# Kernel tuning notes

Measured on AMD Instinct MI355X. Metric: run time of the kernel, lower is better.

The kernel has to match this reference:

```python
import jax, jax.numpy as jnp
import numpy as np
from jax import lax

EPS = 1e-5

def bn(x, g, b):
    # training-mode BatchNorm2d over (N, H, W)
    m = jnp.mean(x, axis=(0, 2, 3), keepdims=True)
    v = jnp.var(x, axis=(0, 2, 3), keepdims=True)
    return (x - m) * lax.rsqrt(v + EPS) * g[None, :, None, None] + b[None, :, None, None]

def conv1x1(x, W):
    # x: [b,c,h,w], W: [o,c]
    return jnp.einsum('bchw,oc->bohw', x, W)

def conv3x3(x, W):
    # W: [o,i,3,3]
    return lax.conv_general_dilated(x, W, (1, 1), 'SAME',
                                    dimension_numbers=('NCHW', 'OIHW', 'NCHW'))

def lga(x, Wqkv, Wproj, g, b):
    # LinearGlobalAttention: O(N) global attention
    bsz, c, h, w = x.shape
    qkv = conv1x1(x, Wqkv)                       # [b, 3c, h, w]
    q, k, v = jnp.split(qkv, 3, axis=1)
    q = q.reshape(bsz, c, h * w)                 # [b, c, N]
    k = jax.nn.softmax(k.reshape(bsz, c, h * w), axis=-1)
    v = v.reshape(bsz, c, h * w)
    ctx = jnp.einsum('bcn,bdn->bcd', k, v)       # [b, c, c]
    out = jnp.einsum('bcd,bcn->bdn', ctx, q)     # context^T @ q -> [b, c, N]
    out = out.reshape(bsz, c, h, w)
    return jax.nn.relu(bn(conv1x1(out, Wproj), g, b))


def setup_inputs() -> dict:
    key = jax.random.key(0)
    ks = jax.random.split(key, 12)
    B, Cin, Cout, H, W = 16, 128, 256, 64, 64
    wd = Cout // 4  # branch width = 64
    sc = 0.05
    inp = {
        'x': jax.random.normal(ks[0], (B, Cin, H, W), jnp.float32),
        'W_sc': jax.random.normal(ks[1], (Cout, Cin), jnp.float32) * sc,
        'g_sc': jnp.ones((Cout,), jnp.float32),
        'b_sc': jnp.zeros((Cout,), jnp.float32),
        'W1': jax.random.normal(ks[2], (Cout, Cin), jnp.float32) * sc,
        'g1': jnp.ones((Cout,), jnp.float32),
        'b1': jnp.zeros((Cout,), jnp.float32),
        'Wb0': jax.random.normal(ks[3], (wd, wd), jnp.float32) * sc,
        'gb0': jnp.ones((wd,), jnp.float32),
        'bb0': jnp.zeros((wd,), jnp.float32),
        'Wb1': jax.random.normal(ks[4], (wd, wd, 3, 3), jnp.float32) * sc,
        'gb1': jnp.ones((wd,), jnp.float32),
        'bb1': jnp.zeros((wd,), jnp.float32),
        'Wqkv2': jax.random.normal(ks[5], (3 * wd, wd), jnp.float32) * sc,
        'Wproj2': jax.random.normal(ks[6], (wd, wd), jnp.float32) * sc,
        'ga2': jnp.ones((wd,), jnp.float32),
        'ba2': jnp.zeros((wd,), jnp.float32),
        'Wqkv3': jax.random.normal(ks[7], (3 * wd, wd), jnp.float32) * sc,
        'Wproj3': jax.random.normal(ks[8], (wd, wd), jnp.float32) * sc,
        'ga3': jnp.ones((wd,), jnp.float32),
        'ba3': jnp.zeros((wd,), jnp.float32),
        'W2': jax.random.normal(ks[9], (Cout, Cout), jnp.float32) * sc,
        'g2': jnp.ones((Cout,), jnp.float32),
        'b2': jnp.zeros((Cout,), jnp.float32),
    }
    return inp


def reference(x, W_sc, g_sc, b_sc, W1, g1, b1,
              Wb0, gb0, bb0, Wb1, gb1, bb1,
              Wqkv2, Wproj2, ga2, ba2,
              Wqkv3, Wproj3, ga3, ba3,
              W2, g2, b2):
    residual = bn(conv1x1(x, W_sc), g_sc, b_sc)
    h = jax.nn.relu(bn(conv1x1(x, W1), g1, b1))      # [b, 256, H, W]
    s0, s1, s2, s3 = jnp.split(h, 4, axis=1)          # width = 64 each
    o0 = jax.nn.relu(bn(conv1x1(s0, Wb0), gb0, bb0))  # k=1 branch
    o1 = jax.nn.relu(bn(conv3x3(s1, Wb1), gb1, bb1))  # k=3 branch
    o2 = lga(s2, Wqkv2, Wproj2, ga2, ba2)             # k=5 -> attention
    o3 = lga(s3, Wqkv3, Wproj3, ga3, ba3)             # k=7 -> attention
    out = jnp.concatenate([o0, o1, o2, o3], axis=1)
    out = bn(conv1x1(out, W2), g2, b2) + residual
    return jax.nn.relu(out)
```

## Files before the change

kernel.cpp:

```cpp
#include <hip/hip_runtime.h>
#include <hip/hip_bf16.h>

using bf16 = __hip_bfloat16;
typedef __bf16 bf16v8 __attribute__((ext_vector_type(8)));
typedef float f32x4 __attribute__((ext_vector_type(4)));

#define HW 4096
#define ROWS 65536
#define BRSTRIDE 4194304

#define AS1 const __attribute__((address_space(1))) void*
#define AS3 __attribute__((address_space(3))) void*

__global__ void r4_cvt_w(const float* __restrict__ Wsc, const float* __restrict__ W1,
                         const float* __restrict__ Wb0,
                         const float* __restrict__ Wqkv2, const float* __restrict__ Wqkv3,
                         const float* __restrict__ W2, bf16* __restrict__ wbase,
                         float* __restrict__ stats) {
    int i = blockIdx.x * 256 + threadIdx.x;
    if (i < 2048) stats[i] = 0.f;
    const float* s; int off;
    if      (i < 32768)  { s = Wsc;   off = i; }
    else if (i < 65536)  { s = W1;    off = i - 32768; }
    else if (i < 69632)  { s = Wb0;   off = i - 65536; }
    else if (i < 81920)  { s = Wqkv2; off = i - 69632; }
    else if (i < 94208)  { s = Wqkv3; off = i - 81920; }
    else                 { s = W2;    off = i - 94208; }
    wbase[i] = __float2bfloat16(s[off]);
}

__global__ void r4_cvt_x(const float* __restrict__ x, bf16* __restrict__ xT) {
    __shared__ bf16 tile[64 * 65];
    int b = blockIdx.z, c0 = blockIdx.y * 64, n0 = blockIdx.x * 64;
    int t = threadIdx.x;
    for (int i = 0; i < 16; i++) {
        int idx = i * 256 + t;
        int cc = idx >> 6, nn = idx & 63;
        tile[nn * 65 + cc] = __float2bfloat16(x[((size_t)(b * 128 + c0 + cc)) * HW + n0 + nn]);
    }
    __syncthreads();
    for (int i = 0; i < 16; i++) {
        int idx = i * 256 + t;
        int nn = idx >> 6, cc = idx & 63;
        xT[((size_t)(b * HW + n0 + nn)) * 128 + c0 + cc] = tile[nn * 65 + cc];
    }
}

__global__ void r4_pack3(const float* __restrict__ w, bf16* __restrict__ wp) {
    int i = blockIdx.x * 256 + threadIdx.x;
    int tap = i / 4096, rem = i % 4096;
    int o = rem >> 6, c = rem & 63;
    wp[i] = __float2bfloat16(w[(size_t)(o * 64 + c) * 9 + tap]);
}

__global__ __launch_bounds__(256) void r10_act(bf16* __restrict__ buf,
        const float* __restrict__ sums,
        const float* __restrict__ g0, const float* __restrict__ b0,
        const float* __restrict__ g1, const float* __restrict__ b1,
        const float* __restrict__ g2, const float* __restrict__ b2,
        const float* __restrict__ g3, const float* __restrict__ b3,
        int quarter) {
    __shared__ float scS[256], shS[256];
    int t = threadIdx.x;
    {
        const float *gp, *bp; int ci;
        if (quarter) {
            int qi = t >> 6; ci = t & 63;
            gp = qi == 0 ? g0 : qi == 1 ? g1 : qi == 2 ? g2 : g3;
            bp = qi == 0 ? b0 : qi == 1 ? b1 : qi == 2 ? b2 : b3;
        } else { gp = g0; bp = b0; ci = t; }
        float mean = sums[t] * (1.f / 65536.f);
        float var  = sums[256 + t] * (1.f / 65536.f) - mean * mean;
        float s = gp[ci] * rsqrtf(var + 1e-5f);
        scS[t] = s;
        shS[t] = bp[ci] - mean * s;
    }
    __syncthreads();
    long base = (long)blockIdx.x * 8192;
    int c0 = (t & 31) * 8;
#pragma unroll
    for (int i = 0; i < 4; i++) {
        long e = base + i * 2048 + t * 8;
        bf16v8 v = *(const bf16v8*)&buf[e];
#pragma unroll
        for (int j = 0; j < 8; j++) {
            float f = (float)v[j] * scS[c0 + j] + shS[c0 + j];
            v[j] = (__bf16)fmaxf(f, 0.f);
        }
        *(bf16v8*)&buf[e] = v;
    }
}

template <int KK>
__global__ __launch_bounds__(256) void ga_gemm(
        const bf16* __restrict__ A, int a_stride,
        const bf16* __restrict__ W, int w_stride,
        bf16* __restrict__ out0, bf16* __restrict__ out1, int split,
        int out_stride,
        float* __restrict__ stat0, float* __restrict__ stat1,
        int scol0, int scol1) {
    __shared__ bf16 shmem[128 * 136];
    __shared__ float sredS[256], sredQ[256];
    bf16* As = shmem;
    bf16* Ws = shmem + 8192;

    int t = threadIdx.x;
    int wave = t >> 6, lane = t & 63;
    int lo = lane & 15, quad = lane >> 4;
    int wr = wave >> 1, wc = wave & 1;
    int b = blockIdx.z;
    long grow = (long)b * HW + blockIdx.x * 128;
    int o0 = blockIdx.y * 128;
    const bf16* Wb = W + (long)o0 * w_stride;

    f32x4 acc[4][4];
#pragma unroll
    for (int m = 0; m < 4; m++)
#pragma unroll
        for (int n = 0; n < 4; n++) acc[m][n] = (f32x4){0.f, 0.f, 0.f, 0.f};

#pragma unroll
    for (int ph = 0; ph < KK / 64; ph++) {
        int k0 = ph * 64;
#pragma unroll
        for (int j = 0; j < 4; j++) {
            int i = j * 4 + wave;
            int ci = i * 64 + lane;
            int R = ci >> 3, cc = ci & 7;
            int sw = ((cc ^ (R & 7)) << 3);
            __builtin_amdgcn_global_load_lds(
                (AS1)(A + (grow + R) * (long)a_stride + k0 + sw),
                (AS3)(As + i * 512), 16, 0, 0);
            __builtin_amdgcn_global_load_lds(
                (AS1)(Wb + (long)R * w_stride + k0 + sw),
                (AS3)(Ws + i * 512), 16, 0, 0);
        }
        asm volatile("s_waitcnt vmcnt(0)" ::: "memory");
        __syncthreads();
#pragma unroll
        for (int ks = 0; ks < 64; ks += 32) {
            int kk = (ks >> 3) + quad;
            bf16v8 av[4], wv[4];
#pragma unroll
            for (int m = 0; m < 4; m++) {
                int R = wr * 64 + m * 16 + lo;
                av[m] = *(const bf16v8*)&As[R * 64 + ((kk ^ (R & 7)) << 3)];
            }
#pragma unroll
            for (int n = 0; n < 4; n++) {
                int R = wc * 64 + n * 16 + lo;
                wv[n] = *(const bf16v8*)&Ws[R * 64 + ((kk ^ (R & 7)) << 3)];
            }
#pragma unroll
            for (int m = 0; m < 4; m++)
#pragma unroll
                for (int n = 0; n < 4; n++)
                    acc[m][n] = __builtin_amdgcn_mfma_f32_16x16x32_bf16(av[m], wv[n], acc[m][n], 0, 0, 0);
        }
        __syncthreads();
    }

    bf16* Ot = shmem;
#pragma unroll
    for (int m = 0; m < 4; m++)
#pragma unroll
        for (int n = 0; n < 4; n++)
#pragma unroll
            for (int r = 0; r < 4; r++)
                Ot[(wr * 64 + m * 16 + quad * 4 + r) * 136 + wc * 64 + n * 16 + lo] =
                    __float2bfloat16(acc[m][n][r]);
    __syncthreads();
    bool low = o0 < split;
    bf16* op = low ? out0 : out1;
    int oc0 = low ? o0 : o0 - split;
#pragma unroll
    for (int i = 0; i < 8; i++) {
        int u = i * 256 + t;
        int lr = u >> 4, cg = u & 15;
        *(bf16v8*)&op[(grow + lr) * (long)out_stride + oc0 + cg * 8] =
            *(const bf16v8*)&Ot[lr * 136 + cg * 8];
    }
    if (stat0) {
        int c = t & 127, half = t >> 7;
        float s = 0.f, q = 0.f;
#pragma unroll
        for (int r = 0; r < 64; r++) {
            float v = __bfloat162float(Ot[(half * 64 + r) * 136 + c]);
            s += v; q += v * v;
        }
        sredS[t] = s; sredQ[t] = q;
        __syncthreads();
        if (t < 128) {
            float ss = sredS[t] + sredS[t + 128];
            float qq = sredQ[t] + sredQ[t + 128];
            float* st = low ? stat0 : stat1;
            int ci = (low ? scol0 + o0 : scol1 + o0 - split) + c;
            atomicAdd(&st[ci], ss);
            atomicAdd(&st[256 + ci], qq);
        }
    }
}

__global__ __launch_bounds__(256) void gq_gemm(
        const bf16* __restrict__ y1,
        const bf16* __restrict__ wq2, const bf16* __restrict__ wq3,
        const bf16* __restrict__ wb0,
        bf16* __restrict__ qs, bf16* __restrict__ ks, bf16* __restrict__ vs,
        bf16* __restrict__ obuf, float* __restrict__ stats) {
    __shared__ bf16 shmem[256 * 64 + 64 * 64];
    __shared__ float sredS[256], sredQ[256];
    bf16* As = shmem;
    bf16* Ws = shmem + 256 * 64;

    int t = threadIdx.x;
    int wave = t >> 6, lane = t & 63;
    int lo = lane & 15, quad = lane >> 4;
    int b = blockIdx.z, y = blockIdx.y;
    long grow = (long)b * HW + blockIdx.x * 256;

    const bf16* Ab; const bf16* Wb; bf16* outp; int ostride; float* st;
    if (y == 6) {
        Ab = y1; Wb = wb0; outp = obuf; ostride = 256; st = stats;
    } else {
        int br = y / 3, sel = y - br * 3;
        Ab = y1 + 128 + br * 64;
        Wb = (br ? wq3 : wq2) + sel * 4096;
        outp = (sel == 0 ? qs : sel == 1 ? ks : vs) + (long)br * BRSTRIDE;
        ostride = 64; st = nullptr;
    }

    f32x4 acc[4][4];
#pragma unroll
    for (int m = 0; m < 4; m++)
#pragma unroll
        for (int n = 0; n < 4; n++) acc[m][n] = (f32x4){0.f, 0.f, 0.f, 0.f};

#pragma unroll
    for (int j = 0; j < 8; j++) {
        int ci = (j * 4 + wave) * 64 + lane;
        int R = ci >> 3, cc = ci & 7;
        __builtin_amdgcn_global_load_lds(
            (AS1)(Ab + (grow + R) * 256L + ((cc ^ (R & 7)) << 3)),
            (AS3)(As + (j * 4 + wave) * 512), 16, 0, 0);
    }
#pragma unroll
    for (int j = 0; j < 2; j++) {
        int ci = (j * 4 + wave) * 64 + lane;
        int R = ci >> 3, cc = ci & 7;
        __builtin_amdgcn_global_load_lds(
            (AS1)(Wb + R * 64 + ((cc ^ (R & 7)) << 3)),
            (AS3)(Ws + (j * 4 + wave) * 512), 16, 0, 0);
    }
    asm volatile("s_waitcnt vmcnt(0)" ::: "memory");
    __syncthreads();

#pragma unroll
    for (int ks_ = 0; ks_ < 64; ks_ += 32) {
        bf16v8 av[4], wv[4];
#pragma unroll
        for (int m = 0; m < 4; m++) {
            int R = wave * 64 + m * 16 + lo;
            av[m] = *(const bf16v8*)&As[R * 64 + ((((ks_ >> 3) + quad) ^ (R & 7)) << 3)];
        }
#pragma unroll
        for (int n = 0; n < 4; n++) {
            int o = n * 16 + lo;
            wv[n] = *(const bf16v8*)&Ws[o * 64 + ((((ks_ >> 3) + quad) ^ (o & 7)) << 3)];
        }
#pragma unroll
        for (int m = 0; m < 4; m++)
#pragma unroll
            for (int n = 0; n < 4; n++)
                acc[m][n] = __builtin_amdgcn_mfma_f32_16x16x32_bf16(av[m], wv[n], acc[m][n], 0, 0, 0);
    }
    __syncthreads();

    bf16* Ot = shmem;
#pragma unroll
    for (int m = 0; m < 4; m++)
#pragma unroll
        for (int n = 0; n < 4; n++)
#pragma unroll
            for (int r = 0; r < 4; r++)
                Ot[(wave * 64 + m * 16 + quad * 4 + r) * 72 + n * 16 + lo] =
                    __float2bfloat16(acc[m][n][r]);
    __syncthreads();
#pragma unroll
    for (int i = 0; i < 8; i++) {
        int u = i * 256 + t;
        int lr = u >> 3, cg = u & 7;
        *(bf16v8*)&outp[(grow + lr) * (long)ostride + cg * 8] =
            *(const bf16v8*)&Ot[lr * 72 + cg * 8];
    }
    if (st) {
        int c = t & 63, qtr = t >> 6;
        float s = 0.f, q = 0.f;
#pragma unroll
        for (int r = 0; r < 64; r++) {
            float v = __bfloat162float(Ot[(qtr * 64 + r) * 72 + c]);
            s += v; q += v * v;
        }
        sredS[t] = s; sredQ[t] = q;
        __syncthreads();
        if (t < 64) {
            float ss = sredS[t] + sredS[t + 64] + sredS[t + 128] + sredS[t + 192];
            float qq = sredQ[t] + sredQ[t + 64] + sredQ[t + 128] + sredQ[t + 192];
            atomicAdd(&st[t], ss);
            atomicAdd(&st[256 + t], qq);
        }
    }
}

__global__ __launch_bounds__(256) void gp_gemm(
        const bf16* __restrict__ qs, const bf16* __restrict__ M,
        bf16* __restrict__ obuf, float* __restrict__ stats) {
    __shared__ bf16 shmem[256 * 64 + 64 * 64];
    __shared__ float sredS[256], sredQ[256];
    bf16* As = shmem;
    bf16* Ws = shmem + 256 * 64;

    int t = threadIdx.x;
    int wave = t >> 6, lane = t & 63;
    int lo = lane & 15, quad = lane >> 4;
    int b = blockIdx.z, y = blockIdx.y;
    long grow = (long)b * HW + blockIdx.x * 256;
    const bf16* Ab = qs + (long)y * BRSTRIDE;
    const bf16* Wb = M + y * 65536 + (long)b * 4096;
    int oc0 = 128 + y * 64;

    f32x4 acc[4][4];
#pragma unroll
    for (int m = 0; m < 4; m++)
#pragma unroll
        for (int n = 0; n < 4; n++) acc[m][n] = (f32x4){0.f, 0.f, 0.f, 0.f};

#pragma unroll
    for (int j = 0; j < 8; j++) {
        int ci = (j * 4 + wave) * 64 + lane;
        int R = ci >> 3, cc = ci & 7;
        __builtin_amdgcn_global_load_lds(
            (AS1)(Ab + (grow + R) * 64L + ((cc ^ (R & 7)) << 3)),
            (AS3)(As + (j * 4 + wave) * 512), 16, 0, 0);
    }
#pragma unroll
    for (int j = 0; j < 2; j++) {
        int ci = (j * 4 + wave) * 64 + lane;
        int R = ci >> 3, cc = ci & 7;
        __builtin_amdgcn_global_load_lds(
            (AS1)(Wb + R * 64 + ((cc ^ (R & 7)) << 3)),
            (AS3)(Ws + (j * 4 + wave) * 512), 16, 0, 0);
    }
    asm volatile("s_waitcnt vmcnt(0)" ::: "memory");
    __syncthreads();

#pragma unroll
    for (int ks_ = 0; ks_ < 64; ks_ += 32) {
        bf16v8 av[4], wv[4];
#pragma unroll
        for (int m = 0; m < 4; m++) {
            int R = wave * 64 + m * 16 + lo;
            av[m] = *(const bf16v8*)&As[R * 64 + ((((ks_ >> 3) + quad) ^ (R & 7)) << 3)];
        }
#pragma unroll
        for (int n = 0; n < 4; n++) {
            int o = n * 16 + lo;
            wv[n] = *(const bf16v8*)&Ws[o * 64 + ((((ks_ >> 3) + quad) ^ (o & 7)) << 3)];
        }
#pragma unroll
        for (int m = 0; m < 4; m++)
#pragma unroll
            for (int n = 0; n < 4; n++)
                acc[m][n] = __builtin_amdgcn_mfma_f32_16x16x32_bf16(av[m], wv[n], acc[m][n], 0, 0, 0);
    }
    __syncthreads();

    bf16* Ot = shmem;
#pragma unroll
    for (int m = 0; m < 4; m++)
#pragma unroll
        for (int n = 0; n < 4; n++)
#pragma unroll
            for (int r = 0; r < 4; r++)
                Ot[(wave * 64 + m * 16 + quad * 4 + r) * 72 + n * 16 + lo] =
                    __float2bfloat16(acc[m][n][r]);
    __syncthreads();
#pragma unroll
    for (int i = 0; i < 8; i++) {
        int u = i * 256 + t;
        int lr = u >> 3, cg = u & 7;
        *(bf16v8*)&obuf[(grow + lr) * 256L + oc0 + cg * 8] =
            *(const bf16v8*)&Ot[lr * 72 + cg * 8];
    }
    {
        int c = t & 63, qtr = t >> 6;
        float s = 0.f, q = 0.f;
#pragma unroll
        for (int r = 0; r < 64; r++) {
            float v = __bfloat162float(Ot[(qtr * 64 + r) * 72 + c]);
            s += v; q += v * v;
        }
        sredS[t] = s; sredQ[t] = q;
        __syncthreads();
        if (t < 64) {
            float ss = sredS[t] + sredS[t + 64] + sredS[t + 128] + sredS[t + 192];
            float qq = sredQ[t] + sredQ[t + 64] + sredQ[t + 128] + sredQ[t + 192];
            atomicAdd(&stats[oc0 + t], ss);
            atomicAdd(&stats[256 + oc0 + t], qq);
        }
    }
}

__global__ __launch_bounds__(256) void r12_conv3(
        const bf16* __restrict__ hT, const bf16* __restrict__ wp,
        bf16* __restrict__ obuf, float* __restrict__ stat) {
    __shared__ bf16 As[6 * 66 * 64];
    __shared__ bf16 Wt[9 * 64 * 64];
    __shared__ float sredS[256], sredQ[256];

    int t = threadIdx.x;
    int wave = t >> 6, lane = t & 63;
    int lo = lane & 15, quad = lane >> 4;
    int b = blockIdx.y, y0 = blockIdx.x * 4;

#pragma unroll
    for (int j = 0; j < 18; j++) {
        int i = j * 4 + wave;
        int ci = i * 64 + lane;
        int tap = ci >> 9, rem = ci & 511, o = rem >> 3, ck = rem & 7;
        __builtin_amdgcn_global_load_lds(
            (AS1)(wp + tap * 4096 + o * 64 + ((ck ^ (o & 7)) << 3)),
            (AS3)(Wt + i * 512), 16, 0, 0);
    }
#pragma unroll
    for (int j = 0; j < 12; j++) {
        int i = j * 4 + wave;
        int row = i >> 3, seg = i & 7;
        int yy = y0 - 1 + row;
        if (yy >= 0 && yy < 64) {
            int xg = seg * 8 + (lane >> 3), ck = lane & 7;
            __builtin_amdgcn_global_load_lds(
                (AS1)(hT + ((long)b * HW + yy * 64 + xg) * 256 + 64 + ((ck ^ (xg & 7)) << 3)),
                (AS3)(As + row * 4224 + 64 + seg * 512), 16, 0, 0);
        } else {
            *(bf16v8*)&As[row * 4224 + 64 + seg * 512 + lane * 8] = (bf16v8){0,0,0,0,0,0,0,0};
        }
    }
    if (t < 96) {
        int yr = t >> 4, side = (t >> 3) & 1, ck = t & 7;
        *(bf16v8*)&As[yr * 4224 + (side ? 65 : 0) * 64 + ck * 8] = (bf16v8){0,0,0,0,0,0,0,0};
    }
    asm volatile("s_waitcnt vmcnt(0)" ::: "memory");
    __syncthreads();

    f32x4 acc[4][4];
#pragma unroll
    for (int m = 0; m < 4; m++)
#pragma unroll
        for (int n = 0; n < 4; n++) acc[m][n] = (f32x4){0.f, 0.f, 0.f, 0.f};

#pragma unroll
    for (int tap = 0; tap < 9; tap++) {
        int dy = tap / 3 - 1, dx = tap % 3 - 1;
        int yr = wave + 1 + dy;
#pragma unroll
        for (int ks8 = 0; ks8 < 8; ks8 += 4) {
            int kk = ks8 + quad;
            bf16v8 wv[4];
#pragma unroll
            for (int ot = 0; ot < 4; ot++) {
                int o = ot * 16 + lo;
                wv[ot] = *(const bf16v8*)&Wt[tap * 4096 + o * 64 + ((kk ^ (o & 7)) << 3)];
            }
#pragma unroll
            for (int m = 0; m < 4; m++) {
                int xp = m * 16 + lo + dx;
                bf16v8 av = *(const bf16v8*)&As[yr * 4224 + (xp + 1) * 64 + ((kk ^ (xp & 7)) << 3)];
#pragma unroll
                for (int ot = 0; ot < 4; ot++)
                    acc[m][ot] = __builtin_amdgcn_mfma_f32_16x16x32_bf16(av, wv[ot], acc[m][ot], 0, 0, 0);
            }
        }
    }
    __syncthreads();

    bf16* Ot = As;
#pragma unroll
    for (int m = 0; m < 4; m++)
#pragma unroll
        for (int ot = 0; ot < 4; ot++)
#pragma unroll
            for (int r = 0; r < 4; r++)
                Ot[(wave * 64 + m * 16 + quad * 4 + r) * 72 + ot * 16 + lo] =
                    __float2bfloat16(acc[m][ot][r]);
    __syncthreads();

    long grow = (long)b * HW + y0 * 64;
#pragma unroll
    for (int i = 0; i < 8; i++) {
        int u = i * 256 + t;
        int lr = u >> 3, cg = u & 7;
        *(bf16v8*)&obuf[(grow + lr) * 256 + 64 + cg * 8] = *(const bf16v8*)&Ot[lr * 72 + cg * 8];
    }
    {
        int c = t & 63, qtr = t >> 6;
        float s = 0.f, q = 0.f;
#pragma unroll
        for (int r = 0; r < 64; r++) {
            float v = __bfloat162float(Ot[(qtr * 64 + r) * 72 + c]);
            s += v; q += v * v;
        }
        sredS[t] = s; sredQ[t] = q;
        __syncthreads();
        if (t < 64) {
            float ss = sredS[t] + sredS[t + 64] + sredS[t + 128] + sredS[t + 192];
            float qq = sredQ[t] + sredQ[t + 64] + sredQ[t + 128] + sredQ[t + 192];
            atomicAdd(&stat[64 + t], ss);
            atomicAdd(&stat[256 + 64 + t], qq);
        }
    }
}

__global__ __launch_bounds__(256) void r14_softctx(
        const bf16* __restrict__ ks_t, const bf16* __restrict__ vs_t,
        float* __restrict__ ctx_p, float* __restrict__ lpart) {
    __shared__ bf16 Ks[64 * 136];
    __shared__ bf16 Vs[64 * 136];
    __shared__ float red[32 * 64];
    int t = threadIdx.x;
    int wave = t >> 6, lane = t & 63;
    int lo = lane & 15, quad = lane >> 4;
    int b = blockIdx.y, bx = blockIdx.x, z = blockIdx.z;
    const bf16* kb = ks_t + (long)z * BRSTRIDE;
    const bf16* vb = vs_t + (long)z * BRSTRIDE;

    f32x4 acc[4];
#pragma unroll
    for (int ot = 0; ot < 4; ot++) acc[ot] = (f32x4){0.f, 0.f, 0.f, 0.f};
    float sm[8];
#pragma unroll
    for (int j = 0; j < 8; j++) sm[j] = 0.f;

    for (int it = 0; it < 2; it++) {
        long n0 = ((long)bx * 2 + it) * 128;
        __syncthreads();
#pragma unroll
        for (int sub = 0; sub < 4; sub++) {
            int r = sub * 32 + (t >> 3), cg = t & 7;
            long row = (long)b * HW + n0 + r;
            bf16v8 k8 = *(const bf16v8*)(kb + row * 64 + cg * 8);
            bf16v8 v8 = *(const bf16v8*)(vb + row * 64 + cg * 8);
#pragma unroll
            for (int j = 0; j < 8; j++) {
                int c = cg * 8 + j;
                float e = expf((float)k8[j]);
                sm[j] += e;
                Ks[c * 136 + r] = __float2bfloat16(e);
                Vs[c * 136 + r] = (bf16)v8[j];
            }
        }
        __syncthreads();
#pragma unroll
        for (int ks = 0; ks < 128; ks += 32) {
            bf16v8 av = *(const bf16v8*)&Ks[(wave * 16 + lo) * 136 + ks + quad * 8];
#pragma unroll
            for (int ot = 0; ot < 4; ot++) {
                bf16v8 bv = *(const bf16v8*)&Vs[(ot * 16 + lo) * 136 + ks + quad * 8];
                acc[ot] = __builtin_amdgcn_mfma_f32_16x16x32_bf16(av, bv, acc[ot], 0, 0, 0);
            }
        }
    }
    long blk = ((long)z * 16 + b) * 16 + bx;
#pragma unroll
    for (int ot = 0; ot < 4; ot++) {
#pragma unroll
        for (int r = 0; r < 4; r++) {
            int c = wave * 16 + quad * 4 + r;
            int d = ot * 16 + lo;
            ctx_p[(blk * 64 + c) * 64 + d] = acc[ot][r];
        }
    }
    {
        int rg = t >> 3, cg = t & 7;
#pragma unroll
        for (int j = 0; j < 8; j++) red[rg * 64 + cg * 8 + j] = sm[j];
        __syncthreads();
        if (t < 64) {
            float s = 0.f;
#pragma unroll
            for (int i = 0; i < 32; i++) s += red[i * 64 + t];
            lpart[blk * 64 + t] = s;
        }
    }
}

__global__ __launch_bounds__(256) void r15_mproj(
        const float* __restrict__ Wp2, const float* __restrict__ Wp3,
        const float* __restrict__ ctx_p, const float* __restrict__ lpart,
        bf16* __restrict__ M) {
    __shared__ float ctxS[16 * 68];
    __shared__ float ilS[16];
    int b = blockIdx.x, qq = blockIdx.y, z = blockIdx.z, t = threadIdx.x;
    int e = t & 63, cg = t >> 6;
    const float* Wp = z ? Wp3 : Wp2;
    long zb = (long)z * 16 + b;
#pragma unroll
    for (int i = 0; i < 4; i++) {
        int u = i * 256 + t;
        int c_l = u >> 6, d = u & 63;
        float s = 0.f;
#pragma unroll
        for (int p = 0; p < 16; p++)
            s += ctx_p[((zb * 16 + p) * 64 + qq * 16 + c_l) * 64 + d];
        ctxS[c_l * 68 + d] = s;
    }
    if (t < 16) {
        float l = 0.f;
#pragma unroll
        for (int p = 0; p < 16; p++)
            l += lpart[(zb * 16 + p) * 64 + qq * 16 + t];
        ilS[t] = 1.f / l;
    }
    float wreg[64];
#pragma unroll
    for (int i = 0; i < 16; i++) {
        float4 v = *(const float4*)&Wp[e * 64 + i * 4];
        wreg[i * 4 + 0] = v.x; wreg[i * 4 + 1] = v.y;
        wreg[i * 4 + 2] = v.z; wreg[i * 4 + 3] = v.w;
    }
    __syncthreads();
#pragma unroll
    for (int ci = 0; ci < 4; ci++) {
        int c_l = cg * 4 + ci;
        float a = 0.f;
#pragma unroll
        for (int dg = 0; dg < 16; dg++) {
            float4 cv = *(const float4*)&ctxS[c_l * 68 + dg * 4];
            a += wreg[dg * 4 + 0] * cv.x + wreg[dg * 4 + 1] * cv.y
               + wreg[dg * 4 + 2] * cv.z + wreg[dg * 4 + 3] * cv.w;
        }
        M[(long)z * 65536 + (long)b * 4096 + e * 64 + qq * 16 + c_l] =
            __float2bfloat16(a * ilS[c_l]);
    }
}

__global__ void r6_final(const bf16* __restrict__ y2, const bf16* __restrict__ ysc,
                         const float* __restrict__ s2sums, const float* __restrict__ scsums,
                         const float* __restrict__ g2, const float* __restrict__ b2,
                         const float* __restrict__ gsc, const float* __restrict__ bsc,
                         float* __restrict__ out) {
    __shared__ float lo_[64 * 65];
    __shared__ float sc2[64], sh2[64], scc[64], shc[64];
    int b = blockIdx.z, c0 = blockIdx.y * 64, n0 = blockIdx.x * 64;
    int t = threadIdx.x;
    if (t < 64) {
        int ch = c0 + t;
        float m2 = s2sums[ch] * (1.f / 65536.f);
        float v2 = s2sums[256 + ch] * (1.f / 65536.f) - m2 * m2;
        float s = g2[ch] * rsqrtf(v2 + 1e-5f);
        sc2[t] = s; sh2[t] = b2[ch] - m2 * s;
        float mc = scsums[ch] * (1.f / 65536.f);
        float vc = scsums[256 + ch] * (1.f / 65536.f) - mc * mc;
        float s2_ = gsc[ch] * rsqrtf(vc + 1e-5f);
        scc[t] = s2_; shc[t] = bsc[ch] - mc * s2_;
    }
    __syncthreads();
    for (int half = 0; half < 2; half++) {
        int r = half * 32 + (t >> 3), cc = (t & 7) * 8;
        long row = (long)b * HW + n0 + r;
        bf16v8 a8 = *(const bf16v8*)&y2[row * 256 + c0 + cc];
        bf16v8 s8 = *(const bf16v8*)&ysc[row * 256 + c0 + cc];
#pragma unroll
        for (int j = 0; j < 8; j++) {
            int c = cc + j;
            float v = (float)a8[j] * sc2[c] + sh2[c] + (float)s8[j] * scc[c] + shc[c];
            lo_[c * 65 + r] = fmaxf(v, 0.f);
        }
    }
    __syncthreads();
    for (int i = 0; i < 16; i++) {
        int idx = i * 256 + t; int c = idx >> 6, r = idx & 63;
        out[((long)b * 256 + c0 + c) * HW + n0 + r] = lo_[c * 65 + r];
    }
}

extern "C" void kernel_launch(void* const* d_in, const int* in_sizes, int n_in,
                              void* d_out, int out_size, void* d_ws, size_t ws_size,
                              hipStream_t stream) {
    const float* x     = (const float*)d_in[0];
    const float* Wsc   = (const float*)d_in[1];
    const float* gsc   = (const float*)d_in[2];
    const float* bsc   = (const float*)d_in[3];
    const float* W1    = (const float*)d_in[4];
    const float* g1    = (const float*)d_in[5];
    const float* b1    = (const float*)d_in[6];
    const float* Wb0   = (const float*)d_in[7];
    const float* gb0   = (const float*)d_in[8];
    const float* bb0   = (const float*)d_in[9];
    const float* Wb1   = (const float*)d_in[10];
    const float* gb1   = (const float*)d_in[11];
    const float* bb1   = (const float*)d_in[12];
    const float* Wqkv2 = (const float*)d_in[13];
    const float* Wproj2= (const float*)d_in[14];
    const float* ga2   = (const float*)d_in[15];
    const float* ba2   = (const float*)d_in[16];
    const float* Wqkv3 = (const float*)d_in[17];
    const float* Wproj3= (const float*)d_in[18];
    const float* ga3   = (const float*)d_in[19];
    const float* ba3   = (const float*)d_in[20];
    const float* W2    = (const float*)d_in[21];
    const float* g2    = (const float*)d_in[22];
    const float* b2    = (const float*)d_in[23];

    char* ws = (char*)d_ws;
    float* stats = (float*)ws;
    bf16*  M     = (bf16*)(ws + 32768);
    bf16*  wbase = (bf16*)(ws + 294912);
    bf16*  wsc_b = wbase;
    bf16*  wb0_b = wbase + 65536;
    bf16*  wq2_b = wbase + 69632;
    bf16*  wq3_b = wbase + 81920;
    bf16*  w2_b  = wbase + 94208;
    bf16*  wb1p  = (bf16*)(ws + 614400);
    bf16*  xT    = (bf16*)(ws + 1048576);
    bf16*  vs    = (bf16*)(ws + 1048576);
    bf16*  ysc   = (bf16*)(ws + 17825792);
    bf16*  y1    = (bf16*)(ws + 51380224);
    float* ctx_p = (float*)(ws + 51380224);
    float* lpart = (float*)(ws + 51380224 + 8388608);
    bf16*  y2    = y1;
    bf16*  obuf  = (bf16*)d_out;
    bf16*  qs    = (bf16*)((char*)d_out + 33554432);
    bf16*  ks    = (bf16*)((char*)d_out + 50331648);

    r4_cvt_w<<<dim3(624), 256, 0, stream>>>(Wsc, W1, Wb0, Wqkv2, Wqkv3, W2, wbase, stats);
    r4_pack3<<<dim3(144), 256, 0, stream>>>(Wb1, wb1p);
    r4_cvt_x<<<dim3(64, 2, 16), 256, 0, stream>>>(x, xT);

    ga_gemm<128><<<dim3(32, 4, 16), 256, 0, stream>>>(
        xT, 128, wsc_b, 128,
        ysc, y1, 256, 256, stats, stats + 512, 0, 0);
    r10_act<<<dim3(2048), 256, 0, stream>>>(y1, stats + 512,
        g1, b1, g1, b1, g1, b1, g1, b1, 0);

    r12_conv3<<<dim3(16, 16), 256, 0, stream>>>(y1, wb1p, obuf, stats + 1024);
    gq_gemm<<<dim3(16, 7, 16), 256, 0, stream>>>(
        y1, wq2_b, wq3_b, wb0_b, qs, ks, vs, obuf, stats + 1024);

    r14_softctx<<<dim3(16, 16, 2), 256, 0, stream>>>(ks, vs, ctx_p, lpart);
    r15_mproj<<<dim3(16, 4, 2), 256, 0, stream>>>(Wproj2, Wproj3, ctx_p, lpart, M);
    gp_gemm<<<dim3(16, 2, 16), 256, 0, stream>>>(qs, M, obuf, stats + 1024);

    r10_act<<<dim3(2048), 256, 0, stream>>>(obuf, stats + 1024,
        gb0, bb0, gb1, bb1, ga2, ba2, ga3, ba3, 1);
    ga_gemm<256><<<dim3(32, 2, 16), 256, 0, stream>>>(
        obuf, 256, w2_b, 256,
        y2, y2, 1 << 28, 256, stats + 1536, stats + 1536, 0, 0);

    r6_final<<<dim3(64, 4, 16), 256, 0, stream>>>(y2, ysc, stats + 1536, stats + 0,
                                                  g2, b2, gsc, bsc, (float*)d_out);
}
```

Before: 291.3 us.

## Fuse BN+ReLU activation passes into consumer GEMM/conv LDS tiles and vectorize transposes

Removes both standalone r10_act passes. The BN scale/shift and ReLU are now applied in shared memory after each tile load inside the consumer kernels: conv3, gq_gemm and the final ga_gemm. The 3x3 weight packing is merged into the weight-conversion kernel, and the input transpose and final output store now use float4 vector accesses. This saves two full read/write sweeps over 32MB activation buffers and two launches, at the cost of extra LDS passes and syncs inside the GEMMs and redundant activation work on tiles that several blocks share.

```diff
diff --git a/kernel.cpp b/kernel.cpp
--- a/kernel.cpp
+++ b/kernel.cpp
@@ -15,79 +15,51 @@
 __global__ void r4_cvt_w(const float* __restrict__ Wsc, const float* __restrict__ W1,
                          const float* __restrict__ Wb0,
                          const float* __restrict__ Wqkv2, const float* __restrict__ Wqkv3,
-                         const float* __restrict__ W2, bf16* __restrict__ wbase,
+                         const float* __restrict__ W2, const float* __restrict__ Wb1,
+                         bf16* __restrict__ wbase, bf16* __restrict__ wp,
                          float* __restrict__ stats) {
     int i = blockIdx.x * 256 + threadIdx.x;
     if (i < 2048) stats[i] = 0.f;
-    const float* s; int off;
-    if      (i < 32768)  { s = Wsc;   off = i; }
-    else if (i < 65536)  { s = W1;    off = i - 32768; }
-    else if (i < 69632)  { s = Wb0;   off = i - 65536; }
-    else if (i < 81920)  { s = Wqkv2; off = i - 69632; }
-    else if (i < 94208)  { s = Wqkv3; off = i - 81920; }
-    else                 { s = W2;    off = i - 94208; }
-    wbase[i] = __float2bfloat16(s[off]);
+    if (i < 159744) {
+        const float* s; int off;
+        if      (i < 32768)  { s = Wsc;   off = i; }
+        else if (i < 65536)  { s = W1;    off = i - 32768; }
+        else if (i < 69632)  { s = Wb0;   off = i - 65536; }
+        else if (i < 81920)  { s = Wqkv2; off = i - 69632; }
+        else if (i < 94208)  { s = Wqkv3; off = i - 81920; }
+        else                 { s = W2;    off = i - 94208; }
+        wbase[i] = __float2bfloat16(s[off]);
+    } else {
+        int k = i - 159744;
+        int tap = k / 4096, rem = k % 4096;
+        int o = rem >> 6, c = rem & 63;
+        wp[k] = __float2bfloat16(Wb1[(size_t)(o * 64 + c) * 9 + tap]);
+    }
 }
 
 __global__ void r4_cvt_x(const float* __restrict__ x, bf16* __restrict__ xT) {
     __shared__ bf16 tile[64 * 65];
     int b = blockIdx.z, c0 = blockIdx.y * 64, n0 = blockIdx.x * 64;
     int t = threadIdx.x;
-    for (int i = 0; i < 16; i++) {
+#pragma unroll
+    for (int i = 0; i < 4; i++) {
         int idx = i * 256 + t;
-        int cc = idx >> 6, nn = idx & 63;
-        tile[nn * 65 + cc] = __float2bfloat16(x[((size_t)(b * 128 + c0 + cc)) * HW + n0 + nn]);
-    }
-    __syncthreads();
-    for (int i = 0; i < 16; i++) {
-        int idx = i * 256 + t;
-        int nn = idx >> 6, cc = idx & 63;
-        xT[((size_t)(b * HW + n0 + nn)) * 128 + c0 + cc] = tile[nn * 65 + cc];
-    }
-}
-
-__global__ void r4_pack3(const float* __restrict__ w, bf16* __restrict__ wp) {
-    int i = blockIdx.x * 256 + threadIdx.x;
-    int tap = i / 4096, rem = i % 4096;
-    int o = rem >> 6, c = rem & 63;
-    wp[i] = __float2bfloat16(w[(size_t)(o * 64 + c) * 9 + tap]);
-}
-
-__global__ __launch_bounds__(256) void r10_act(bf16* __restrict__ buf,
-        const float* __restrict__ sums,
-        const float* __restrict__ g0, const float* __restrict__ b0,
-        const float* __restrict__ g1, const float* __restrict__ b1,
-        const float* __restrict__ g2, const float* __restrict__ b2,
-        const float* __restrict__ g3, const float* __restrict__ b3,
-        int quarter) {
-    __shared__ float scS[256], shS[256];
-    int t = threadIdx.x;
-    {
-        const float *gp, *bp; int ci;
-        if (quarter) {
-            int qi = t >> 6; ci = t & 63;
-            gp = qi == 0 ? g0 : qi == 1 ? g1 : qi == 2 ? g2 : g3;
-            bp = qi == 0 ? b0 : qi == 1 ? b1 : qi == 2 ? b2 : b3;
-        } else { gp = g0; bp = b0; ci = t; }
-        float mean = sums[t] * (1.f / 65536.f);
-        float var  = sums[256 + t] * (1.f / 65536.f) - mean * mean;
-        float s = gp[ci] * rsqrtf(var + 1e-5f);
-        scS[t] = s;
-        shS[t] = bp[ci] - mean * s;
-    }
-    __syncthreads();
-    long base = (long)blockIdx.x * 8192;
-    int c0 = (t & 31) * 8;
-#pragma unroll
-    for (int i = 0; i < 4; i++) {
-        long e = base + i * 2048 + t * 8;
-        bf16v8 v = *(const bf16v8*)&buf[e];
-#pragma unroll
-        for (int j = 0; j < 8; j++) {
-            float f = (float)v[j] * scS[c0 + j] + shS[c0 + j];
-            v[j] = (__bf16)fmaxf(f, 0.f);
-        }
-        *(bf16v8*)&buf[e] = v;
+        int cc = idx >> 4, n4 = (idx & 15) * 4;
+        float4 v = *(const float4*)&x[((size_t)(b * 128 + c0 + cc)) * HW + n0 + n4];
+        tile[(n4 + 0) * 65 + cc] = __float2bfloat16(v.x);
+        tile[(n4 + 1) * 65 + cc] = __float2bfloat16(v.y);
+        tile[(n4 + 2) * 65 + cc] = __float2bfloat16(v.z);
+        tile[(n4 + 3) * 65 + cc] = __float2bfloat16(v.w);
+    }
+    __syncthreads();
+#pragma unroll
+    for (int i = 0; i < 2; i++) {
+        int u = i * 256 + t;
+        int nn = u >> 3, p = u & 7;
+        bf16v8 v;
+#pragma unroll
+        for (int j = 0; j < 8; j++) v[j] = (__bf16)tile[nn * 65 + p * 8 + j];
+        *(bf16v8*)&xT[((size_t)(b * HW + n0 + nn)) * 128 + c0 + p * 8] = v;
     }
 }
 
@@ -98,9 +70,15 @@
         bf16* __restrict__ out0, bf16* __restrict__ out1, int split,
         int out_stride,
         float* __restrict__ stat0, float* __restrict__ stat1,
-        int scol0, int scol1) {
+        int scol0, int scol1,
+        const float* __restrict__ tsums,
+        const float* __restrict__ tg0, const float* __restrict__ tb0,
+        const float* __restrict__ tg1, const float* __restrict__ tb1,
+        const float* __restrict__ tg2, const float* __restrict__ tb2,
+        const float* __restrict__ tg3, const float* __restrict__ tb3) {
     __shared__ bf16 shmem[128 * 136];
     __shared__ float sredS[256], sredQ[256];
+    __shared__ float scS[256], shS[256];
     bf16* As = shmem;
     bf16* Ws = shmem + 8192;
 
@@ -112,6 +90,16 @@
     long grow = (long)b * HW + blockIdx.x * 128;
     int o0 = blockIdx.y * 128;
     const bf16* Wb = W + (long)o0 * w_stride;
+
+    if (tsums) {
+        int qi = t >> 6, ci = t & 63;
+        const float* gp = qi == 0 ? tg0 : qi == 1 ? tg1 : qi == 2 ? tg2 : tg3;
+        const float* bp = qi == 0 ? tb0 : qi == 1 ? tb1 : qi == 2 ? tb2 : tb3;
+        float mean = tsums[t] * (1.f / 65536.f);
+        float var  = tsums[256 + t] * (1.f / 65536.f) - mean * mean;
+        float s = gp[ci] * rsqrtf(var + 1e-5f);
+        scS[t] = s; shS[t] = bp[ci] - mean * s;
+    }
 
     f32x4 acc[4][4];
 #pragma unroll
@@ -137,6 +125,22 @@
         }
         asm volatile("s_waitcnt vmcnt(0)" ::: "memory");
         __syncthreads();
+        if (tsums) {
+#pragma unroll
+            for (int i = 0; i < 4; i++) {
+                int ci = i * 256 + t;
+                int R = ci >> 3, p = ci & 7;
+                int chb = k0 + ((p ^ (R & 7)) << 3);
+                bf16v8 v = *(const bf16v8*)&As[R * 64 + p * 8];
+#pragma unroll
+                for (int j = 0; j < 8; j++) {
+                    float f = (float)v[j] * scS[chb + j] + shS[chb + j];
+                    v[j] = (__bf16)fmaxf(f, 0.f);
+                }
+                *(bf16v8*)&As[R * 64 + p * 8] = v;
+            }
+            __syncthreads();
+        }
 #pragma unroll
         for (int ks = 0; ks < 64; ks += 32) {
             int kk = (ks >> 3) + quad;
@@ -206,9 +210,12 @@
         const bf16* __restrict__ wq2, const bf16* __restrict__ wq3,
         const bf16* __restrict__ wb0,
         bf16* __restrict__ qs, bf16* __restrict__ ks, bf16* __restrict__ vs,
-        bf16* __restrict__ obuf, float* __restrict__ stats) {
+        bf16* __restrict__ obuf, float* __restrict__ stats,
+        const float* __restrict__ asums,
+        const float* __restrict__ g1, const float* __restrict__ b1) {
     __shared__ bf16 shmem[256 * 64 + 64 * 64];
     __shared__ float sredS[256], sredQ[256];
+    __shared__ float scS[64], shS[64];
     bf16* As = shmem;
     bf16* Ws = shmem + 256 * 64;
 
@@ -218,15 +225,23 @@
     int b = blockIdx.z, y = blockIdx.y;
     long grow = (long)b * HW + blockIdx.x * 256;
 
-    const bf16* Ab; const bf16* Wb; bf16* outp; int ostride; float* st;
+    const bf16* Ab; const bf16* Wb; bf16* outp; int ostride; float* st; int col0;
     if (y == 6) {
-        Ab = y1; Wb = wb0; outp = obuf; ostride = 256; st = stats;
+        Ab = y1; Wb = wb0; outp = obuf; ostride = 256; st = stats; col0 = 0;
     } else {
         int br = y / 3, sel = y - br * 3;
-        Ab = y1 + 128 + br * 64;
+        col0 = 128 + br * 64;
+        Ab = y1 + col0;
         Wb = (br ? wq3 : wq2) + sel * 4096;
         outp = (sel == 0 ? qs : sel == 1 ? ks : vs) + (long)br * BRSTRIDE;
         ostride = 64; st = nullptr;
+    }
+    if (t < 64) {
+        int ch = col0 + t;
+        float mean = asums[ch] * (1.f / 65536.f);
+        float var  = asums[256 + ch] * (1.f / 65536.f) - mean * mean;
+        float s = g1[ch] * rsqrtf(var + 1e-5f);
+        scS[t] = s; shS[t] = b1[ch] - mean * s;
     }
 
     f32x4 acc[4][4];
@@ -252,6 +267,20 @@
             (AS3)(Ws + (j * 4 + wave) * 512), 16, 0, 0);
     }
     asm volatile("s_waitcnt vmcnt(0)" ::: "memory");
+    __syncthreads();
+#pragma unroll
+    for (int i = 0; i < 8; i++) {
+        int ci = i * 256 + t;
+        int R = ci >> 3, p = ci & 7;
+        int chb = (p ^ (R & 7)) << 3;
+        bf16v8 v = *(const bf16v8*)&As[R * 64 + p * 8];
+#pragma unroll
+        for (int j = 0; j < 8; j++) {
+            float f = (float)v[j] * scS[chb + j] + shS[chb + j];
+            v[j] = (__bf16)fmaxf(f, 0.f);
+        }
+        *(bf16v8*)&As[R * 64 + p * 8] = v;
+    }
     __syncthreads();
 
 #pragma unroll
@@ -412,15 +441,26 @@
 
 __global__ __launch_bounds__(256) void r12_conv3(
         const bf16* __restrict__ hT, const bf16* __restrict__ wp,
-        bf16* __restrict__ obuf, float* __restrict__ stat) {
+        bf16* __restrict__ obuf, float* __restrict__ stat,
+        const float* __restrict__ asums,
+        const float* __restrict__ g1, const float* __restrict__ b1) {
     __shared__ bf16 As[6 * 66 * 64];
     __shared__ bf16 Wt[9 * 64 * 64];
     __shared__ float sredS[256], sredQ[256];
+    __shared__ float scS[64], shS[64];
 
     int t = threadIdx.x;
     int wave = t >> 6, lane = t & 63;
     int lo = lane & 15, quad = lane >> 4;
     int b = blockIdx.y, y0 = blockIdx.x * 4;
+
+    if (t < 64) {
+        int ch = 64 + t;
+        float mean = asums[ch] * (1.f / 65536.f);
+        float var  = asums[256 + ch] * (1.f / 65536.f) - mean * mean;
+        float s = g1[ch] * rsqrtf(var + 1e-5f);
+        scS[t] = s; shS[t] = b1[ch] - mean * s;
+    }
 
 #pragma unroll
     for (int j = 0; j < 18; j++) {
@@ -450,6 +490,24 @@
         *(bf16v8*)&As[yr * 4224 + (side ? 65 : 0) * 64 + ck * 8] = (bf16v8){0,0,0,0,0,0,0,0};
     }
     asm volatile("s_waitcnt vmcnt(0)" ::: "memory");
+    __syncthreads();
+#pragma unroll
+    for (int i = 0; i < 12; i++) {
+        int ci = i * 256 + t;
+        int row = ci >> 9, rem = ci & 511;
+        int xg = rem >> 3, p = rem & 7;
+        int yy = y0 - 1 + row;
+        if (yy >= 0 && yy < 64) {
+            int chb = (p ^ (xg & 7)) << 3;
+            bf16v8 v = *(const bf16v8*)&As[row * 4224 + (xg + 1) * 64 + p * 8];
+#pragma unroll
+            for (int j = 0; j < 8; j++) {
+                float f = (float)v[j] * scS[chb + j] + shS[chb + j];
+                v[j] = (__bf16)fmaxf(f, 0.f);
+            }
+            *(bf16v8*)&As[row * 4224 + (xg + 1) * 64 + p * 8] = v;
+        }
+    }
     __syncthreads();
 
     f32x4 acc[4][4];
@@ -677,9 +735,16 @@
         }
     }
     __syncthreads();
-    for (int i = 0; i < 16; i++) {
-        int idx = i * 256 + t; int c = idx >> 6, r = idx & 63;
-        out[((long)b * 256 + c0 + c) * HW + n0 + r] = lo_[c * 65 + r];
+#pragma unroll
+    for (int i = 0; i < 4; i++) {
+        int idx = i * 256 + t;
+        int c = idx >> 4, r4 = (idx & 15) * 4;
+        float4 w;
+        w.x = lo_[c * 65 + r4 + 0];
+        w.y = lo_[c * 65 + r4 + 1];
+        w.z = lo_[c * 65 + r4 + 2];
+        w.w = lo_[c * 65 + r4 + 3];
+        *(float4*)&out[((long)(b * 256 + c0 + c)) * HW + n0 + r4] = w;
     }
 }
 
@@ -732,29 +797,29 @@
     bf16*  qs    = (bf16*)((char*)d_out + 33554432);
     bf16*  ks    = (bf16*)((char*)d_out + 50331648);
 
-    r4_cvt_w<<<dim3(624), 256, 0, stream>>>(Wsc, W1, Wb0, Wqkv2, Wqkv3, W2, wbase, stats);
-    r4_pack3<<<dim3(144), 256, 0, stream>>>(Wb1, wb1p);
+    r4_cvt_w<<<dim3(768), 256, 0, stream>>>(Wsc, W1, Wb0, Wqkv2, Wqkv3, W2, Wb1,
+                                            wbase, wb1p, stats);
     r4_cvt_x<<<dim3(64, 2, 16), 256, 0, stream>>>(x, xT);
 
     ga_gemm<128><<<dim3(32, 4, 16), 256, 0, stream>>>(
         xT, 128, wsc_b, 128,
-        ysc, y1, 256, 256, stats, stats + 512, 0, 0);
-    r10_act<<<dim3(2048), 256, 0, stream>>>(y1, stats + 512,
-        g1, b1, g1, b1, g1, b1, g1, b1, 0);
-
-    r12_conv3<<<dim3(16, 16), 256, 0, stream>>>(y1, wb1p, obuf, stats + 1024);
+        ysc, y1, 256, 256, stats, stats + 512, 0, 0,
+        nullptr, nullptr, nullptr, nullptr, nullptr, nullptr, nullptr, nullptr, nullptr);
+
+    r12_conv3<<<dim3(16, 16), 256, 0, stream>>>(y1, wb1p, obuf, stats + 1024,
+                                                stats + 512, g1, b1);
     gq_gemm<<<dim3(16, 7, 16), 256, 0, stream>>>(
-        y1, wq2_b, wq3_b, wb0_b, qs, ks, vs, obuf, stats + 1024);
+        y1, wq2_b, wq3_b, wb0_b, qs, ks, vs, obuf, stats + 1024,
+        stats + 512, g1, b1);
 
     r14_softctx<<<dim3(16, 16, 2), 256, 0, stream>>>(ks, vs, ctx_p, lpart);
     r15_mproj<<<dim3(16, 4, 2), 256, 0, stream>>>(Wproj2, Wproj3, ctx_p, lpart, M);
     gp_gemm<<<dim3(16, 2, 16), 256, 0, stream>>>(qs, M, obuf, stats + 1024);
 
-    r10_act<<<dim3(2048), 256, 0, stream>>>(obuf, stats + 1024,
-        gb0, bb0, gb1, bb1, ga2, ba2, ga3, ba3, 1);
     ga_gemm<256><<<dim3(32, 2, 16), 256, 0, stream>>>(
         obuf, 256, w2_b, 256,
-        y2, y2, 1 << 28, 256, stats + 1536, stats + 1536, 0, 0);
+        y2, y2, 1 << 28, 256, stats + 1536, stats + 1536, 0, 0,
+        stats + 1024, gb0, bb0, gb1, bb1, ga2, ba2, ga3, ba3);
 
     r6_final<<<dim3(64, 4, 16), 256, 0, stream>>>(y2, ysc, stats + 1536, stats + 0,
                                                   g2, b2, gsc, bsc, (float*)d_out);
```

New measurement: 280.8 us. 3.6% less time.
